# Kernel tuning notes

Measured on AMD Instinct MI355X. Metric: run time of the kernel, lower is better.

## Reference

```python
import jax, jax.numpy as jnp
import numpy as np

NGRAM = 2
NUM_HEADS = 16
NUM_BUCKETS = 32
EMBED_DIM = 1024
REAL_T = 512
BSZ = 4


def setup_inputs() -> dict:
    key = jax.random.key(0)
    ks = jax.random.split(key, 10)
    tgt_len = (1 + NGRAM) * REAL_T
    E, H, NB = EMBED_DIM, NUM_HEADS, NUM_BUCKETS
    w = 0.02
    return {
        "query": jax.random.normal(ks[0], (tgt_len, BSZ, E), jnp.float32),
        "self_attn_mask": jnp.zeros((REAL_T, REAL_T), jnp.float32),
        "ngram_mask_matrix": jnp.zeros((NGRAM, REAL_T, 2 * REAL_T), jnp.float32),
        "i_buckets_main_stream": jax.random.randint(ks[1], (BSZ, REAL_T, REAL_T), 0, NB, jnp.int32),
        "i_bucket_relative_stream": jax.random.randint(ks[2], (BSZ, REAL_T, 2 * REAL_T), 0, NB, jnp.int32),
        "in_proj_weight": jax.random.normal(ks[3], (3 * E, E), jnp.float32) * w,
        "in_proj_bias": jnp.zeros((3 * E,), jnp.float32),
        "out_proj_weight": jax.random.normal(ks[4], (E, E), jnp.float32) * w,
        "out_proj_bias": jnp.zeros((E,), jnp.float32),
        "relative_weight": jax.random.normal(ks[5], (NB * H, E), jnp.float32) * w,
        "relative_bias": jnp.zeros((NB * H,), jnp.float32),
    }


def _forward(query, self_attn_mask, ngram_mask_matrix,
             ib_main, ib_rel,
             in_proj_weight, in_proj_bias, out_proj_weight, out_proj_bias,
             relative_weight, relative_bias):
    tgt_len, bsz, E = query.shape
    H, n = NUM_HEADS, NGRAM
    hd = E // H
    nb = relative_weight.shape[0] // H
    T = tgt_len // (1 + n)
    scaling = hd ** -0.5

    # fused qkv projection
    qkv = query @ in_proj_weight.T + in_proj_bias  # [tgt, B, 3E]
    q, k, v = jnp.split(qkv, 3, axis=-1)
    q = q * scaling

    def to_bh(x):  # [tgt, B, E] -> [B*H, tgt, hd]
        return x.reshape(tgt_len, bsz * H, hd).transpose(1, 0, 2)
    q, k, v = to_bh(q), to_bh(k), to_bh(v)

    h_main = query[:T]                                  # [T, B, E]
    h_pred = query[T:].reshape(n, T, bsz, E)            # [n, T, B, E]
    q_main, k_main, v_main = q[:, :T], k[:, :T], v[:, :T]            # [BH, T, hd]
    def pred(x):  # [BH, n*T, hd] -> [n, BH, T, hd]
        return x[:, T:].reshape(bsz * H, n, T, hd).transpose(1, 0, 2, 3)
    q_pred, k_pred, v_pred = pred(q), pred(k), pred(v)

    # ---- main stream ----
    aw_main = jnp.einsum('bth,bsh->bts', q_main, k_main)  # [BH, T, T]
    # relative bias: per-token bucket values gathered by bucket index
    vals_main = h_main.transpose(1, 0, 2) @ relative_weight.T + relative_bias  # [B, T, nb*H]
    vals_main = vals_main.reshape(bsz, T, nb, H).transpose(0, 3, 1, 2)         # [B, H, T, nb]
    ib = jnp.broadcast_to(ib_main[:, None].astype(jnp.int32), (bsz, H, T, T))
    rel_main = jnp.take_along_axis(vals_main, ib, axis=-1).reshape(bsz * H, T, T)
    aw_main = aw_main + rel_main + self_attn_mask[None]
    p_main = jax.nn.softmax(aw_main, axis=-1)
    attn_main = jnp.einsum('bts,bsh->bth', p_main, v_main)  # [BH, T, hd]
    attn_main = attn_main.transpose(1, 0, 2).reshape(T, bsz, E)

    # ---- ngram predict streams ----
    k_ng = jnp.concatenate([jnp.broadcast_to(k_main[None], (n,) + k_main.shape), k_pred], axis=2)  # [n, BH, 2T, hd]
    v_ng = jnp.concatenate([jnp.broadcast_to(v_main[None], (n,) + v_main.shape), v_pred], axis=2)
    aw_ng = jnp.einsum('nbtc,nbsc->nbts', q_pred, k_ng)  # [n, BH, T, 2T]

    vals_ng = h_pred.transpose(0, 2, 1, 3) @ relative_weight.T + relative_bias  # [n, B, T, nb*H]
    vals_ng = vals_ng.reshape(n, bsz, T, nb, H).transpose(0, 1, 4, 2, 3)        # [n, B, H, T, nb]
    ibr = jnp.broadcast_to(ib_rel[None, :, None].astype(jnp.int32), (n, bsz, H, T, 2 * T))
    rel_ng = jnp.take_along_axis(vals_ng, ibr, axis=-1).reshape(n, bsz * H, T, 2 * T)
    aw_ng = aw_ng + rel_ng + ngram_mask_matrix[:, None]
    p_ng = jax.nn.softmax(aw_ng, axis=-1)
    attn_ng = jnp.einsum('nbts,nbsc->nbtc', p_ng, v_ng)  # [n, BH, T, hd]
    attn_ng = attn_ng.transpose(0, 2, 1, 3).reshape(n * T, bsz, E)

    attn = jnp.concatenate([attn_main, attn_ng], axis=0)  # [tgt, B, E]
    return attn @ out_proj_weight.T + out_proj_bias


def reference(query, self_attn_mask, ngram_mask_matrix,
              i_buckets_main_stream, i_bucket_relative_stream,
              in_proj_weight, in_proj_bias, out_proj_weight, out_proj_bias,
              relative_weight, relative_bias):
    return _forward(query, self_attn_mask, ngram_mask_matrix,
                    i_buckets_main_stream, i_bucket_relative_stream,
                    in_proj_weight, in_proj_bias, out_proj_weight, out_proj_bias,
                    relative_weight, relative_bias)
```

## Files before the change

kernel.cpp:

```cpp
#include <hip/hip_runtime.h>

#define TSEQ 512
#define BSZN 4
#define NH 16
#define NBN 32
#define EMB 1024
#define HD 64
#define TGT 1536
#define MROWS 6144
#define LOG2E 1.44269504088896f

typedef unsigned short ushort_t;
typedef __bf16 bf8 __attribute__((ext_vector_type(8)));
typedef __bf16 bf2_t __attribute__((ext_vector_type(2)));
typedef ushort_t u16x8v __attribute__((ext_vector_type(8)));
typedef float f32x4 __attribute__((ext_vector_type(4)));

__device__ __forceinline__ unsigned short f2bf(float f) {
  return __builtin_bit_cast(unsigned short, (__bf16)f);
}

__device__ __forceinline__ float bf2f(unsigned short u) {
  return __builtin_bit_cast(float, (unsigned int)u << 16);
}

__device__ __forceinline__ unsigned int packbf(float a, float b) {
  bf2_t t;
  t[0] = (__bf16)a;
  t[1] = (__bf16)b;
  return __builtin_bit_cast(unsigned int, t);
}

__device__ __forceinline__ void gload16(const void* g, void* l) {
  __builtin_amdgcn_global_load_lds(
      (const __attribute__((address_space(1))) void*)g,
      (__attribute__((address_space(3))) void*)l, 16, 0, 0);
}

__device__ __forceinline__ f32x4 mfma_bf16(bf8 a, bf8 b, f32x4 c) {
  return __builtin_amdgcn_mfma_f32_16x16x32_bf16(a, b, c, 0, 0, 0);
}

__device__ __forceinline__ float lanebcast(float v, int srclane) {
  return __builtin_bit_cast(float,
      __builtin_amdgcn_ds_bpermute(srclane * 4, __builtin_bit_cast(int, v)));
}

__global__ void prep_all_kernel(const float* __restrict__ q, const float* __restrict__ win,
                                const float* __restrict__ wout, const float* __restrict__ wrel,
                                const int* __restrict__ ibm, const int* __restrict__ ibr,
                                const float* __restrict__ mm, const float* __restrict__ mng,
                                ushort_t* __restrict__ qo, ushort_t* __restrict__ wino,
                                ushort_t* __restrict__ wouto, ushort_t* __restrict__ wrelo,
                                unsigned int* __restrict__ cm, unsigned int* __restrict__ cng) {
  const int i = blockIdx.x * blockDim.x + threadIdx.x;
  const int n0 = 1572864, n1 = 786432, n2 = 262144, n3 = 131072;
  const int ncvt = n0 + n1 + n2 + n3;
  const int nm = 262144, nr = 1048576;
  if (i < ncvt) {
    const float* src;
    ushort_t* dst;
    int off;
    if (i < n0) { src = q; dst = qo; off = i; }
    else if (i < n0 + n1) { src = win; dst = wino; off = i - n0; }
    else if (i < n0 + n1 + n2) { src = wout; dst = wouto; off = i - n0 - n1; }
    else { src = wrel; dst = wrelo; off = i - n0 - n1 - n2; }
    const float4 v = reinterpret_cast<const float4*>(src)[off];
    ushort4 o;
    o.x = f2bf(v.x); o.y = f2bf(v.y); o.z = f2bf(v.z); o.w = f2bf(v.w);
    reinterpret_cast<ushort4*>(dst)[off] = o;
  } else if (i < ncvt + nm) {
    const int f = (i - ncvt) * 4;
    const int4 ib = *reinterpret_cast<const int4*>(ibm + f);
    const float4 mk = *reinterpret_cast<const float4*>(mm + (f & 262143));
    uint4 o;
    o.x = ((unsigned int)f2bf(mk.x * LOG2E) << 16) | ((unsigned int)ib.x & 31u);
    o.y = ((unsigned int)f2bf(mk.y * LOG2E) << 16) | ((unsigned int)ib.y & 31u);
    o.z = ((unsigned int)f2bf(mk.z * LOG2E) << 16) | ((unsigned int)ib.z & 31u);
    o.w = ((unsigned int)f2bf(mk.w * LOG2E) << 16) | ((unsigned int)ib.w & 31u);
    *reinterpret_cast<uint4*>(cm + f) = o;
  } else if (i < ncvt + nm + nr) {
    const int f = (i - ncvt - nm) * 4;
    const int ib_off = ((f >> 20) << 19) + (f & 524287);
    const int mk_off = f & 1048575;
    const int4 ib = *reinterpret_cast<const int4*>(ibr + ib_off);
    const float4 mk = *reinterpret_cast<const float4*>(mng + mk_off);
    uint4 o;
    o.x = ((unsigned int)f2bf(mk.x * LOG2E) << 16) | ((unsigned int)ib.x & 31u);
    o.y = ((unsigned int)f2bf(mk.y * LOG2E) << 16) | ((unsigned int)ib.y & 31u);
    o.z = ((unsigned int)f2bf(mk.z * LOG2E) << 16) | ((unsigned int)ib.z & 31u);
    o.w = ((unsigned int)f2bf(mk.w * LOG2E) << 16) | ((unsigned int)ib.w & 31u);
    *reinterpret_cast<uint4*>(cng + f) = o;
  }
}

template <int MODE>
__global__ __launch_bounds__(256) void gemm_bt(
    const ushort_t* __restrict__ A, const ushort_t* __restrict__ B,
    const float* __restrict__ bias, float* __restrict__ Cf,
    ushort_t* __restrict__ Qo, ushort_t* __restrict__ Ko, ushort_t* __restrict__ Vto,
    const ushort_t* __restrict__ B2, const float* __restrict__ bias2,
    ushort_t* __restrict__ VMo, int M, int N, int K) {
  __shared__ ushort_t lds[16384];
  ushort_t* lA = lds;
  ushort_t* lB = lds + 8192;

  const int tid = threadIdx.x;
  const int lane = tid & 63;
  const int wid = tid >> 6;
  const int l15 = lane & 15, l4 = lane >> 4;

  int bm, bn;
  {
    const int n = blockIdx.x;
    const int xcd = n & 7;
    const int idx = n >> 3;
    if (MODE == 0) {
      const int chunk = idx / 42;
      const int w = idx - chunk * 42;
      bm = xcd * 6 + (w % 6);
      bn = chunk * 7 + (w / 6);
    } else {
      bm = xcd * 6 + (idx % 6);
      bn = idx / 6;
    }
  }
  const int wm = (wid >> 1) * 64, wn = (wid & 1) * 64;
  const bool isrel = (MODE == 0) && (bn >= 24);

  f32x4 acc[4][4] = {};

  const int r8 = tid >> 3;
  const int c8 = ((tid & 7) ^ (r8 & 7)) * 8;
  const ushort_t* Ag = A + (size_t)(bm * 128 + r8) * K + c8;
  const ushort_t* Bg = isrel ? B2 + (size_t)((bn - 24) * 128 + r8) * K + c8
                             : B + (size_t)(bn * 128 + r8) * K + c8;
  ushort_t* lAp = lA + tid * 8;
  ushort_t* lBp = lB + tid * 8;

  for (int kt = 0; kt < K; kt += 64) {
    __syncthreads();
#pragma unroll
    for (int i = 0; i < 4; ++i) {
      gload16(Ag + (size_t)i * 32 * K + kt, lAp + i * 2048);
      gload16(Bg + (size_t)i * 32 * K + kt, lBp + i * 2048);
    }
    __syncthreads();
#pragma unroll
    for (int k0 = 0; k0 < 2; ++k0) {
      bf8 af[4], bv[4];
#pragma unroll
      for (int mi = 0; mi < 4; ++mi) {
        const int row = wm + mi * 16 + l15;
        const int slot = (k0 * 4 + l4) ^ (row & 7);
        af[mi] = *reinterpret_cast<const bf8*>(lA + row * 64 + slot * 8);
      }
#pragma unroll
      for (int ni = 0; ni < 4; ++ni) {
        const int row = wn + ni * 16 + l15;
        const int slot = (k0 * 4 + l4) ^ (row & 7);
        bv[ni] = *reinterpret_cast<const bf8*>(lB + row * 64 + slot * 8);
      }
      __builtin_amdgcn_s_setprio(1);
#pragma unroll
      for (int mi = 0; mi < 4; ++mi)
#pragma unroll
        for (int ni = 0; ni < 4; ++ni)
          acc[mi][ni] = mfma_bf16(af[mi], bv[ni], acc[mi][ni]);
      __builtin_amdgcn_s_setprio(0);
    }
  }

  if (MODE == 0 && bn < 16) {
    __syncthreads();
    char* tb = reinterpret_cast<char*>(lds);
    const float scale = (bn < 8) ? (0.125f * LOG2E) : 1.f;
#pragma unroll
    for (int ni = 0; ni < 4; ++ni) {
      const int colloc = wn + ni * 16 + l15;
      const float bc = bias[bn * 128 + colloc];
#pragma unroll
      for (int mi = 0; mi < 4; ++mi) {
        f32x4 v = acc[mi][ni];
#pragma unroll
        for (int r = 0; r < 4; ++r) {
          const int row_loc = wm + mi * 16 + l4 * 4 + r;
          const int byteoff = row_loc * 256 + ((colloc * 2) ^ ((row_loc & 7) << 4));
          *reinterpret_cast<ushort_t*>(tb + byteoff) = f2bf((v[r] + bc) * scale);
        }
      }
    }
    __syncthreads();
    ushort_t* dst = (bn < 8) ? Qo : Ko;
    const int tglob0 = bm * 32;
#pragma unroll
    for (int p = 0; p < 2; ++p) {
      const int pair = wid * 2 + p;
      const int bb = pair >> 1;
      const int hl = pair & 1;
      const int h = (bn & 7) * 2 + hl;
      const int bh = bb * NH + h;
#pragma unroll
      for (int ii = 0; ii < 4; ++ii) {
        const int t_loc = ii * 8 + (lane >> 3);
        const int row_loc = t_loc * 4 + bb;
        const int byteoff = row_loc * 256 +
            ((hl * 128 + (lane & 7) * 16) ^ ((row_loc & 7) << 4));
        const u16x8v val = *reinterpret_cast<const u16x8v*>(tb + byteoff);
        *reinterpret_cast<u16x8v*>(
            dst + ((size_t)bh * TGT + tglob0 + t_loc) * HD + (lane & 7) * 8) = val;
      }
    }
    return;
  }

  if (MODE == 0 && bn >= 16 && bn < 24) {
    __syncthreads();
    char* tb = reinterpret_cast<char*>(lds);
#pragma unroll
    for (int ni = 0; ni < 4; ++ni) {
      const int colloc = wn + ni * 16 + l15;
      const float bc = bias[bn * 128 + colloc];
      const unsigned int swz = (colloc & 7) << 4;
#pragma unroll
      for (int mi = 0; mi < 4; ++mi) {
        const int t_loc = (wm >> 2) + mi * 4 + l4;
        f32x4 v = acc[mi][ni];
#pragma unroll
        for (int r = 0; r < 4; ++r) {
          const int byteoff = colloc * 256 + ((r * 64 + t_loc * 2) ^ swz);
          *reinterpret_cast<ushort_t*>(tb + byteoff) = f2bf(v[r] + bc);
        }
      }
    }
    __syncthreads();
    const int tglob0 = bm * 32;
#pragma unroll
    for (int p = 0; p < 2; ++p) {
      const int pair = wid * 2 + p;
      const int bb = pair >> 1;
      const int hl = pair & 1;
      const int hh = (bn - 16) * 2 + hl;
      const int bh = bb * NH + hh;
      const int tch = lane & 3;
#pragma unroll
      for (int ii = 0; ii < 4; ++ii) {
        const int dloc = ii * 16 + (lane >> 2);
        const int colloc = hl * 64 + dloc;
        const int byteoff = colloc * 256 + ((bb * 64 + tch * 16) ^ ((colloc & 7) << 4));
        const u16x8v val = *reinterpret_cast<const u16x8v*>(tb + byteoff);
        *reinterpret_cast<u16x8v*>(
            Vto + ((size_t)bh * HD + dloc) * TGT + tglob0 + tch * 8) = val;
      }
    }
    return;
  }

#pragma unroll
  for (int ni = 0; ni < 4; ++ni) {
    const int colloc = wn + ni * 16 + l15;
    const int col = bn * 128 + colloc;
    const int colrel = (bn - 24) * 128 + colloc;
    const float bc = isrel ? bias2[colrel] : bias[col];
#pragma unroll
    for (int mi = 0; mi < 4; ++mi) {
      const int row0 = bm * 128 + wm + mi * 16 + l4 * 4;
      f32x4 v = acc[mi][ni];
#pragma unroll
      for (int r = 0; r < 4; ++r) {
        const int row = row0 + r;
        float val = v[r] + bc;
        if (MODE == 0) {
          const int hh = colrel & 15, nb = colrel >> 4;
          const int qg = row >> 2, bb2 = row & 3;
          VMo[(((size_t)(bb2 * NH + hh)) * TGT + qg) * NBN + nb] = f2bf(val * LOG2E);
        } else {
          Cf[(size_t)row * N + col] = val;
        }
      }
    }
  }
}

__global__ __launch_bounds__(256, 3) void attn_kernel(
    const ushort_t* __restrict__ Q, const ushort_t* __restrict__ Kb,
    const ushort_t* __restrict__ Vt, const ushort_t* __restrict__ VMh,
    const unsigned int* __restrict__ comb_main, const unsigned int* __restrict__ comb_ng,
    ushort_t* __restrict__ AT) {
  __shared__ unsigned char kbuf[2][8192];
  __shared__ unsigned char vbuf[2][8192];
  __shared__ ushort_t vmt16[4][1088];
  __shared__ unsigned int pbl[4][576];

  const int tid = threadIdx.x;
  const int lane = tid & 63, wid = tid >> 6;
  const int l15 = lane & 15, l4 = lane >> 4;

  const int n = blockIdx.x;
  const int xcd = n & 7;
  const int b = xcd >> 1;
  const int idx = (xcd & 1) * 96 + (n >> 3);
  const int h = idx / 12;
  const int rem = idx - h * 12;
  const int z = rem >> 2;
  const int blk = rem & 3;
  const int g = (z == 0) ? 0 : z - 1;
  const int bh = b * NH + h;
  const int t0 = blk * 128 + wid * 32;
  const int qrow0 = (z == 0) ? t0 : TSEQ + g * TSEQ + t0;
  const int nsb = (z == 0) ? 8 : 16;

  {
    const ushort_t* src = VMh + ((size_t)bh * TGT + qrow0) * NBN;
    ushort_t* dst = vmt16[wid];
#pragma unroll
    for (int half = 0; half < 2; ++half) {
      const u16x8v v = *reinterpret_cast<const u16x8v*>(src + half * 512 + lane * 8);
      const int r = half * 16 + (lane >> 2);
      const int c0 = (lane & 3) * 8;
#pragma unroll
      for (int i = 0; i < 8; ++i) dst[r * 34 + c0 + i] = v[i];
    }
  }

  bf8 qf[2][2];
#pragma unroll
  for (int th = 0; th < 2; ++th)
#pragma unroll
    for (int hf = 0; hf < 2; ++hf)
      qf[th][hf] = *reinterpret_cast<const bf8*>(
          &Q[((size_t)bh * TGT + qrow0 + th * 16 + l15) * HD + hf * 32 + l4 * 8]);

  const unsigned int* cb[2];
  {
    const unsigned int* cbase = (z == 0)
        ? comb_main + (size_t)b * TSEQ * TSEQ
        : comb_ng + (size_t)(b * 2 + g) * TSEQ * (2 * TSEQ);
    const int sstr = (z == 0) ? TSEQ : 2 * TSEQ;
    cb[0] = cbase + (size_t)(t0 + l15) * sstr;
    cb[1] = cbase + (size_t)(t0 + 16 + l15) * sstr;
  }

  float m_run[2] = {-1e30f, -1e30f};
  float l_run[2] = {0.f, 0.f};
  f32x4 oacc[2][4] = {};

  const int r8 = lane >> 3;
  const int swzs = ((lane & 7) ^ r8) << 4;
  const int swzr = (l15 & 7) << 4;

  auto stage = [&](int sb, int bf) {
    const int srow0 = (sb < 8) ? sb * 64 : TSEQ + g * TSEQ + (sb - 8) * 64;
    const ushort_t* ks = Kb + ((size_t)bh * TGT + srow0 + wid * 16 + r8) * HD + (swzs >> 1);
    gload16(ks, &kbuf[bf][wid * 2048 + lane * 16]);
    gload16(ks + 8 * HD, &kbuf[bf][wid * 2048 + 1024 + lane * 16]);
    const ushort_t* vs = Vt + ((size_t)bh * HD + wid * 16 + r8) * TGT + srow0 + (swzs >> 1);
    gload16(vs, &vbuf[bf][wid * 2048 + lane * 16]);
    gload16(vs + 8 * TGT, &vbuf[bf][wid * 2048 + 1024 + lane * 16]);
  };

  stage(0, 0);
  asm volatile("s_waitcnt vmcnt(0)" ::: "memory");
  __builtin_amdgcn_s_barrier();

  int cur = 0;
  for (int sb = 0; sb < nsb; ++sb) {
    const int scol = sb * 64;
    if (sb + 1 < nsb) stage(sb + 1, cur ^ 1);

    const unsigned char* kb = kbuf[cur];
    const unsigned char* vbb = vbuf[cur];

    uint4 cw[2][4];
#pragma unroll
    for (int th = 0; th < 2; ++th) {
      const unsigned int* cwp = cb[th] + scol + l4 * 4;
      cw[th][0] = *reinterpret_cast<const uint4*>(cwp);
      cw[th][1] = *reinterpret_cast<const uint4*>(cwp + 16);
      cw[th][2] = *reinterpret_cast<const uint4*>(cwp + 32);
      cw[th][3] = *reinterpret_cast<const uint4*>(cwp + 48);
    }

    bf8 kf[4][2];
#pragma unroll
    for (int j = 0; j < 4; ++j) {
      const int row = j * 16 + l15;
      kf[j][0] = *reinterpret_cast<const bf8*>(kb + row * 128 + ((l4 * 16) ^ swzr));
      kf[j][1] = *reinterpret_cast<const bf8*>(kb + row * 128 + ((64 + l4 * 16) ^ swzr));
    }
    f32x4 st[2][4];
    __builtin_amdgcn_s_setprio(1);
#pragma unroll
    for (int th = 0; th < 2; ++th)
#pragma unroll
      for (int j = 0; j < 4; ++j) {
        f32x4 s4 = {};
        s4 = mfma_bf16(kf[j][0], qf[th][0], s4);
        s4 = mfma_bf16(kf[j][1], qf[th][1], s4);
        st[th][j] = s4;
      }
    __builtin_amdgcn_s_setprio(0);

#pragma unroll
    for (int th = 0; th < 2; ++th) {
      const ushort_t* vrow = vmt16[wid] + (th * 16 + l15) * 34;
      float vals[4][4];
      float mx = -1e30f;
#pragma unroll
      for (int j = 0; j < 4; ++j) {
        const unsigned int w0 = cw[th][j].x, w1 = cw[th][j].y;
        const unsigned int w2 = cw[th][j].z, w3 = cw[th][j].w;
        vals[j][0] = st[th][j][0] + __builtin_bit_cast(float, w0 & 0xffff0000u) + bf2f(vrow[w0 & 31u]);
        vals[j][1] = st[th][j][1] + __builtin_bit_cast(float, w1 & 0xffff0000u) + bf2f(vrow[w1 & 31u]);
        vals[j][2] = st[th][j][2] + __builtin_bit_cast(float, w2 & 0xffff0000u) + bf2f(vrow[w2 & 31u]);
        vals[j][3] = st[th][j][3] + __builtin_bit_cast(float, w3 & 0xffff0000u) + bf2f(vrow[w3 & 31u]);
        mx = fmaxf(mx, fmaxf(fmaxf(vals[j][0], vals[j][1]), fmaxf(vals[j][2], vals[j][3])));
      }
      mx = fmaxf(mx, __shfl_xor(mx, 16));
      mx = fmaxf(mx, __shfl_xor(mx, 32));

      const float oldm = m_run[th];
      if (!__all(mx - oldm <= 8.f)) {
        const float newm = fmaxf(oldm, mx);
        const float fct = (oldm <= -1e30f) ? 0.f : exp2f(oldm - newm);
        f32x4 rs;
        rs[0] = lanebcast(fct, l4 * 4 + 0);
        rs[1] = lanebcast(fct, l4 * 4 + 1);
        rs[2] = lanebcast(fct, l4 * 4 + 2);
        rs[3] = lanebcast(fct, l4 * 4 + 3);
#pragma unroll
        for (int dt = 0; dt < 4; ++dt) oacc[th][dt] *= rs;
        l_run[th] *= fct;
        m_run[th] = newm;
      }
      const float mref = m_run[th];

      unsigned int pk[4][2];
      float lsum = 0.f;
#pragma unroll
      for (int j = 0; j < 4; ++j) {
        const float p0 = exp2f(vals[j][0] - mref);
        const float p1 = exp2f(vals[j][1] - mref);
        const float p2 = exp2f(vals[j][2] - mref);
        const float p3 = exp2f(vals[j][3] - mref);
        lsum += (p0 + p1) + (p2 + p3);
        pk[j][0] = packbf(p0, p1);
        pk[j][1] = packbf(p2, p3);
      }
      lsum += __shfl_xor(lsum, 16);
      lsum += __shfl_xor(lsum, 32);
      l_run[th] += lsum;

      {
        unsigned int* prow = &pbl[wid][l15 * 36];
#pragma unroll
        for (int j = 0; j < 4; ++j) {
          uint2 w2v;
          w2v.x = pk[j][0];
          w2v.y = pk[j][1];
          *reinterpret_cast<uint2*>(&prow[j * 8 + l4 * 2]) = w2v;
        }
      }
      const unsigned char* pbase = reinterpret_cast<const unsigned char*>(&pbl[wid][0]);
#pragma unroll
      for (int k32 = 0; k32 < 2; ++k32) {
        const bf8 pa = *reinterpret_cast<const bf8*>(
            pbase + l15 * 144 + k32 * 64 + l4 * 16);
        __builtin_amdgcn_s_setprio(1);
#pragma unroll
        for (int dt = 0; dt < 4; ++dt) {
          const bf8 vb = *reinterpret_cast<const bf8*>(
              vbb + (dt * 16 + l15) * 128 + ((k32 * 64 + l4 * 16) ^ swzr));
          oacc[th][dt] = mfma_bf16(pa, vb, oacc[th][dt]);
        }
        __builtin_amdgcn_s_setprio(0);
      }
    }

    asm volatile("s_waitcnt vmcnt(0)" ::: "memory");
    __builtin_amdgcn_s_barrier();
    cur ^= 1;
  }

#pragma unroll
  for (int th = 0; th < 2; ++th) {
    const float linv = 1.f / l_run[th];
    f32x4 bs;
    bs[0] = lanebcast(linv, l4 * 4 + 0);
    bs[1] = lanebcast(linv, l4 * 4 + 1);
    bs[2] = lanebcast(linv, l4 * 4 + 2);
    bs[3] = lanebcast(linv, l4 * 4 + 3);
#pragma unroll
    for (int dt = 0; dt < 4; ++dt) {
#pragma unroll
      for (int r = 0; r < 4; ++r) {
        const int tout = qrow0 + th * 16 + l4 * 4 + r;
        AT[((size_t)tout * BSZN + b) * EMB + h * HD + dt * 16 + l15] =
            f2bf(oacc[th][dt][r] * bs[r]);
      }
    }
  }
}

extern "C" void kernel_launch(void* const* d_in, const int* in_sizes, int n_in,
                              void* d_out, int out_size, void* d_ws, size_t ws_size,
                              hipStream_t stream) {
  const float* query     = (const float*)d_in[0];
  const float* mask_main = (const float*)d_in[1];
  const float* mask_ng   = (const float*)d_in[2];
  const int*   ib_main   = (const int*)d_in[3];
  const int*   ib_rel    = (const int*)d_in[4];
  const float* w_in      = (const float*)d_in[5];
  const float* b_in      = (const float*)d_in[6];
  const float* w_out     = (const float*)d_in[7];
  const float* b_out     = (const float*)d_in[8];
  const float* w_rel     = (const float*)d_in[9];
  const float* b_rel     = (const float*)d_in[10];
  float* out = (float*)d_out;

  ushort_t* qbf    = (ushort_t*)d_ws;
  ushort_t* winbf  = qbf + 6291456;
  ushort_t* woutbf = winbf + 3145728;
  ushort_t* relwbf = woutbf + 1048576;
  ushort_t* Qb     = relwbf + 524288;
  ushort_t* Kbuf   = Qb + 6291456;
  ushort_t* Vtb    = Kbuf + 6291456;
  ushort_t* VMh    = Vtb + 6291456;
  unsigned int* comb_main = (unsigned int*)(VMh + 3145728);
  unsigned int* comb_ng   = comb_main + 1048576;
  ushort_t* AT     = qbf;

  {
    const int total = 2752512 + 262144 + 1048576;
    prep_all_kernel<<<(total + 255) / 256, 256, 0, stream>>>(
        query, w_in, w_out, w_rel, ib_main, ib_rel, mask_main, mask_ng,
        qbf, winbf, woutbf, relwbf, comb_main, comb_ng);
  }

  gemm_bt<0><<<1344, 256, 0, stream>>>(qbf, winbf, b_in, nullptr,
                                       Qb, Kbuf, Vtb, relwbf, b_rel, VMh,
                                       MROWS, 3072, 1024);
  attn_kernel<<<768, 256, 0, stream>>>(Qb, Kbuf, Vtb, VMh, comb_main, comb_ng, AT);
  gemm_bt<2><<<384, 256, 0, stream>>>(AT, woutbf, b_out, out,
                                      nullptr, nullptr, nullptr, nullptr, nullptr,
                                      nullptr, MROWS, 1024, 1024);
}
```

Measured before the change: 189.8 us.

## Double-buffer LDS tiles in GEMM to overlap global loads with MFMA

Splits the GEMM's shared-memory staging into two buffers so the next K-tile's global-to-LDS loads are issued while MFMAs run on the current tile. Each iteration then needs one waitcnt plus barrier instead of two syncthreads. This hides memory latency in the projection GEMMs, at the cost of doubling LDS per block to 64KB, which may cut occupancy. The epilogue barriers are removed, relying on the loop's final barrier.

```diff
diff --git a/kernel.cpp b/kernel.cpp
--- a/kernel.cpp
+++ b/kernel.cpp
@@ -101,9 +101,7 @@
     ushort_t* __restrict__ Qo, ushort_t* __restrict__ Ko, ushort_t* __restrict__ Vto,
     const ushort_t* __restrict__ B2, const float* __restrict__ bias2,
     ushort_t* __restrict__ VMo, int M, int N, int K) {
-  __shared__ ushort_t lds[16384];
-  ushort_t* lA = lds;
-  ushort_t* lB = lds + 8192;
+  __shared__ ushort_t lds[2][16384];
 
   const int tid = threadIdx.x;
   const int lane = tid & 63;
@@ -135,17 +133,27 @@
   const ushort_t* Ag = A + (size_t)(bm * 128 + r8) * K + c8;
   const ushort_t* Bg = isrel ? B2 + (size_t)((bn - 24) * 128 + r8) * K + c8
                              : B + (size_t)(bn * 128 + r8) * K + c8;
-  ushort_t* lAp = lA + tid * 8;
-  ushort_t* lBp = lB + tid * 8;
-
-  for (int kt = 0; kt < K; kt += 64) {
-    __syncthreads();
+
+  auto stage = [&](int kt, int bf) {
+    ushort_t* lAp = lds[bf] + tid * 8;
+    ushort_t* lBp = lds[bf] + 8192 + tid * 8;
 #pragma unroll
     for (int i = 0; i < 4; ++i) {
       gload16(Ag + (size_t)i * 32 * K + kt, lAp + i * 2048);
       gload16(Bg + (size_t)i * 32 * K + kt, lBp + i * 2048);
     }
-    __syncthreads();
+  };
+
+  stage(0, 0);
+  asm volatile("s_waitcnt vmcnt(0)" ::: "memory");
+  __builtin_amdgcn_s_barrier();
+
+  const int NT = K >> 6;
+  int cur = 0;
+  for (int t = 0; t < NT; ++t) {
+    if (t + 1 < NT) stage((t + 1) * 64, cur ^ 1);
+    const ushort_t* lA = lds[cur];
+    const ushort_t* lB = lds[cur] + 8192;
 #pragma unroll
     for (int k0 = 0; k0 < 2; ++k0) {
       bf8 af[4], bv[4];
@@ -169,11 +177,13 @@
           acc[mi][ni] = mfma_bf16(af[mi], bv[ni], acc[mi][ni]);
       __builtin_amdgcn_s_setprio(0);
     }
+    asm volatile("s_waitcnt vmcnt(0)" ::: "memory");
+    __builtin_amdgcn_s_barrier();
+    cur ^= 1;
   }
 
   if (MODE == 0 && bn < 16) {
-    __syncthreads();
-    char* tb = reinterpret_cast<char*>(lds);
+    char* tb = reinterpret_cast<char*>(&lds[0][0]);
     const float scale = (bn < 8) ? (0.125f * LOG2E) : 1.f;
 #pragma unroll
     for (int ni = 0; ni < 4; ++ni) {
@@ -215,8 +225,7 @@
   }
 
   if (MODE == 0 && bn >= 16 && bn < 24) {
-    __syncthreads();
-    char* tb = reinterpret_cast<char*>(lds);
+    char* tb = reinterpret_cast<char*>(&lds[0][0]);
 #pragma unroll
     for (int ni = 0; ni < 4; ++ni) {
       const int colloc = wn + ni * 16 + l15;
```

New measurement: 190.5 us. No clear change (+0.4%).
